# Kernel optimization log

Hardware: AMD Instinct MI355X
Metric: run time of the kernel (lower is better)

## Reference

```python
import jax, jax.numpy as jnp
import numpy as np

IMG = 512; P = 16; C = 3; DIM = 512; DEPTH = 2; HEADS = 8; HD = DIM // HEADS
MLP = 2048; W = 64; NCLS = 1000; B = 8
NPATCH = (IMG // P) ** 2          # 1024
N0 = NPATCH + 1                    # 1025 tokens incl CLS
PAD = (-N0) % (2 * W)              # pad to multiple of 2w (sliding_chunks)
N = N0 + PAD                       # 1152


def _ln(x, w, b):
    m = x.mean(-1, keepdims=True)
    v = jnp.mean((x - m) ** 2, -1, keepdims=True)
    return (x - m) * jax.lax.rsqrt(v + 1e-5) * w + b


def _heads(t):
    b, n, _ = t.shape
    return t.reshape(b, n, HEADS, HD).transpose(0, 2, 1, 3)  # b h n d


def _attn(x, mask, wq, bq, wk, bk, wv, bv, wqg, bqg, wkg, bkg, wvg, bvg):
    b, n, _ = x.shape
    sc = 1.0 / np.sqrt(HD)
    q = _heads(x @ wq + bq) * sc
    k = _heads(x @ wk + bk)
    v = _heads(x @ wv + bv)
    nc = n // W
    qc = q.reshape(b, HEADS, nc, W, HD)

    def chunk3(t):  # gather prev/self/next chunk of keys/values: b h nc 3W d
        tc = t.reshape(b, HEADS, nc, W, HD)
        z = jnp.zeros_like(tc[:, :, :1])
        prev = jnp.concatenate([z, tc[:, :, :-1]], 2)
        nxt = jnp.concatenate([tc[:, :, 1:], z], 2)
        return jnp.concatenate([prev, tc, nxt], 3)

    k3, v3 = chunk3(k), chunk3(v)
    band = jnp.einsum('bhcqd,bhckd->bhcqk', qc, k3)  # b h nc W 3W
    qi = jnp.arange(W)[:, None]
    kk = jnp.arange(3 * W)[None, :]
    rel_ok = jnp.abs(kk - W - qi) <= W               # exact +-w band
    kglob = jnp.arange(nc)[:, None, None] * W + (kk - W)[None]  # nc 1 3W
    in_rng = (kglob >= 0) & (kglob < n)
    kmask = mask[jnp.clip(kglob, 0, n - 1)]
    # keep only real local keys: exclude pad (0) and global (2, handled by gcol)
    keep = rel_ok[None] & in_rng & (kmask == 1.0)    # nc W 3W
    band = jnp.where(keep[None, None], band, -1e9)
    gcol = jnp.einsum('bhnd,bhd->bhn', q, k[:, :, 0])  # attend to global CLS key
    scores = jnp.concatenate([gcol[..., None], band.reshape(b, HEADS, n, 3 * W)], -1)
    a = jax.nn.softmax(scores, -1)                   # b h n (1+3W)
    out = jnp.einsum('bhcqk,bhckd->bhcqd', a[..., 1:].reshape(b, HEADS, nc, W, 3 * W), v3)
    out = out.reshape(b, HEADS, n, HD) + a[..., 0:1] * v[:, :, 0:1]
    # global CLS row attends to everything with its own projections
    qg0 = ((x[:, 0] @ wqg + bqg) * sc).reshape(b, HEADS, HD)
    kg = _heads(x @ wkg + bkg)
    vg = _heads(x @ wvg + bvg)
    gs = jnp.where(mask[None, None] > 0, jnp.einsum('bhd,bhnd->bhn', qg0, kg), -1e9)
    gout = jnp.einsum('bhn,bhnd->bhd', jax.nn.softmax(gs, -1), vg)
    out = out.at[:, :, 0].set(gout)
    return out.transpose(0, 2, 1, 3).reshape(b, n, DIM)


def setup_inputs():
    key = jax.random.key(0)
    ks = iter(jax.random.split(key, 20))

    def w(shape, s=0.02):
        return jax.random.normal(next(ks), shape, jnp.float32) * s

    return {
        'img': jax.random.normal(next(ks), (B, C, IMG, IMG), jnp.float32),
        'patch_w': w((P * P * C, DIM)), 'patch_b': jnp.zeros((DIM,), jnp.float32),
        'cls_tok': jax.random.uniform(next(ks), (1, 1, DIM), jnp.float32),
        'pos_emb': w((1, N0, DIM), 1.0),
        'ln1_w': jnp.ones((DEPTH, DIM), jnp.float32), 'ln1_b': jnp.zeros((DEPTH, DIM), jnp.float32),
        'wq': w((DEPTH, DIM, DIM)), 'bq': jnp.zeros((DEPTH, DIM), jnp.float32),
        'wk': w((DEPTH, DIM, DIM)), 'bk': jnp.zeros((DEPTH, DIM), jnp.float32),
        'wv': w((DEPTH, DIM, DIM)), 'bv': jnp.zeros((DEPTH, DIM), jnp.float32),
        'wqg': w((DEPTH, DIM, DIM)), 'bqg': jnp.zeros((DEPTH, DIM), jnp.float32),
        'wkg': w((DEPTH, DIM, DIM)), 'bkg': jnp.zeros((DEPTH, DIM), jnp.float32),
        'wvg': w((DEPTH, DIM, DIM)), 'bvg': jnp.zeros((DEPTH, DIM), jnp.float32),
        'ln2_w': jnp.ones((DEPTH, DIM), jnp.float32), 'ln2_b': jnp.zeros((DEPTH, DIM), jnp.float32),
        'w1': w((DEPTH, DIM, MLP)), 'b1': jnp.zeros((DEPTH, MLP), jnp.float32),
        'w2': w((DEPTH, MLP, DIM)), 'b2': jnp.zeros((DEPTH, DIM), jnp.float32),
        'head_ln_w': jnp.ones((DIM,), jnp.float32), 'head_ln_b': jnp.zeros((DIM,), jnp.float32),
        'head_w': w((DIM, NCLS)), 'head_b': jnp.zeros((NCLS,), jnp.float32),
    }


def reference(img, patch_w, patch_b, cls_tok, pos_emb, ln1_w, ln1_b, wq, bq, wk, bk,
              wv, bv, wqg, bqg, wkg, bkg, wvg, bvg, ln2_w, ln2_b, w1, b1, w2, b2,
              head_ln_w, head_ln_b, head_w, head_b):
    b = img.shape[0]
    hh = IMG // P
    # b c (h p1) (w p2) -> b (h w) (p1 p2 c)
    x = img.reshape(b, C, hh, P, hh, P).transpose(0, 2, 4, 3, 5, 1).reshape(b, hh * hh, P * P * C)
    x = x @ patch_w + patch_b
    x = jnp.concatenate([jnp.broadcast_to(cls_tok, (b, 1, DIM)), x], 1) + pos_emb
    x = jnp.pad(x, ((0, 0), (0, PAD), (0, 0)))
    mask = jnp.zeros((N,), jnp.float32).at[:N0].set(1.0).at[0].set(2.0)
    for i in range(DEPTH):
        x = x + _attn(_ln(x, ln1_w[i], ln1_b[i]), mask,
                      wq[i], bq[i], wk[i], bk[i], wv[i], bv[i],
                      wqg[i], bqg[i], wkg[i], bkg[i], wvg[i], bvg[i])
        h = jax.nn.gelu(_ln(x, ln2_w[i], ln2_b[i]) @ w1[i] + b1[i], approximate=False)
        x = x + h @ w2[i] + b2[i]
    cls = x[:, 0]  # pool='cls'
    return _ln(cls, head_ln_w, head_ln_b) @ head_w + head_b
```

## Files before the change

### kernel.cpp

```cpp
#include <hip/hip_runtime.h>
#include <hip/hip_bf16.h>
#include <math.h>

typedef __hip_bfloat16 bf16;
typedef float f32x4 __attribute__((ext_vector_type(4)));
typedef short s16x8 __attribute__((ext_vector_type(8)));
typedef unsigned int u32;

#define NB 8
#define NROW 1025
#define MTOT (NB*NROW)
#define DIMD 512
#define NHEAD 8
#define HD 64
#define MLPD 2048
#define QKVN 2560
#define JSTR 1032

__device__ __forceinline__ float b2f(short u) {
    return __builtin_bit_cast(float, (u32)(unsigned short)u << 16);
}
__device__ __forceinline__ unsigned short f2bfbits(float f) {
    __hip_bfloat16 h = __float2bfloat16(f);
    return __builtin_bit_cast(unsigned short, h);
}
__device__ __forceinline__ void g2lds16(const bf16* g, bf16* l) {
    __builtin_amdgcn_global_load_lds((const __attribute__((address_space(1))) u32*)g,
                                     (__attribute__((address_space(3))) u32*)l, 16, 0, 0);
}

__global__ __launch_bounds__(256) void transpose_cvt_L(
    const float* __restrict__ src, bf16* __restrict__ dst, int K, int N, float scale)
{
    __shared__ float t[32][33];
    const int z = blockIdx.z;
    const float* s = src + (size_t)z * K * N;
    bf16* d = dst + (size_t)z * N * K;
    const int n0 = blockIdx.x * 32, k0 = blockIdx.y * 32;
    const int tx = threadIdx.x, ty = threadIdx.y;
#pragma unroll
    for (int i = 0; i < 32; i += 8)
        t[ty + i][tx] = s[(long)(k0 + ty + i) * N + n0 + tx];
    __syncthreads();
#pragma unroll
    for (int i = 0; i < 32; i += 8)
        d[(long)(n0 + ty + i) * K + k0 + tx] = __float2bfloat16(t[tx][ty + i] * scale);
}

__global__ __launch_bounds__(256) void qkvw_t(
    const float* __restrict__ wq, const float* __restrict__ wk, const float* __restrict__ wv,
    const float* __restrict__ wkg, const float* __restrict__ wvg, bf16* __restrict__ qkvT)
{
    __shared__ float t[32][33];
    const int z = blockIdx.z, L = z / 5, s = z % 5;
    const float* srcs[5] = {wq, wk, wv, wkg, wvg};
    const float* src = srcs[s] + (size_t)L * DIMD * DIMD;
    bf16* dst = qkvT + ((size_t)L * QKVN + s * DIMD) * DIMD;
    const float scale = (s == 0) ? 0.125f : 1.f;
    const int n0 = blockIdx.x * 32, k0 = blockIdx.y * 32;
    const int tx = threadIdx.x, ty = threadIdx.y;
#pragma unroll
    for (int i = 0; i < 32; i += 8)
        t[ty + i][tx] = src[(long)(k0 + ty + i) * DIMD + n0 + tx];
    __syncthreads();
#pragma unroll
    for (int i = 0; i < 32; i += 8)
        dst[(long)(n0 + ty + i) * DIMD + k0 + tx] = __float2bfloat16(t[tx][ty + i] * scale);
}

__global__ __launch_bounds__(256) void build_bias(
    const float* __restrict__ bq, const float* __restrict__ bk, const float* __restrict__ bv,
    const float* __restrict__ bkg, const float* __restrict__ bvg, float* __restrict__ outb)
{
    int idx = blockIdx.x * 256 + threadIdx.x;
    if (idx >= 2 * QKVN) return;
    int L = idx / QKVN, c = idx % QKVN;
    int sec = c >> 9, d = c & 511;
    const float* src = (sec == 0) ? bq : (sec == 1) ? bk : (sec == 2) ? bv : (sec == 3) ? bkg : bvg;
    float v = src[L * DIMD + d];
    if (sec == 0) v *= 0.125f;
    outb[idx] = v;
}

__global__ __launch_bounds__(256) void im2col(
    const float* __restrict__ img, bf16* __restrict__ A)
{
    const int idx = blockIdx.x * 256 + threadIdx.x;
    const int pp = idx & 7;
    const int pw = (idx >> 3) & 31;
    const int py = (idx >> 8) & 15;
    const int ph = (idx >> 12) & 31;
    const int b  = idx >> 17;
    const int hh = ph * 16 + py;
    const int w  = pw * 16 + pp * 2;
    const float2 c0 = *(const float2*)(img + (((long)(b * 3 + 0) * 512 + hh) * 512 + w));
    const float2 c1 = *(const float2*)(img + (((long)(b * 3 + 1) * 512 + hh) * 512 + w));
    const float2 c2 = *(const float2*)(img + (((long)(b * 3 + 2) * 512 + hh) * 512 + w));
    const long row = (long)b * 1024 + ph * 32 + pw;
    u32* dst = (u32*)(A + row * 768 + py * 48 + pp * 6);
    dst[0] = (u32)f2bfbits(c0.x) | ((u32)f2bfbits(c1.x) << 16);
    dst[1] = (u32)f2bfbits(c2.x) | ((u32)f2bfbits(c0.y) << 16);
    dst[2] = (u32)f2bfbits(c1.y) | ((u32)f2bfbits(c2.y) << 16);
}

__global__ __launch_bounds__(256) void cls_row(
    const float* __restrict__ cls, const float* __restrict__ pos, float* __restrict__ x)
{
    const int idx = blockIdx.x * 256 + threadIdx.x;
    const int b = idx >> 9, d = idx & 511;
    x[(long)b * NROW * DIMD + d] = cls[d] + pos[d];
}

__global__ __launch_bounds__(256) void ln_fwd(
    const float* __restrict__ x, const float* __restrict__ w,
    const float* __restrict__ bb, bf16* __restrict__ y, int Mrows)
{
    const int row = blockIdx.x * 4 + (threadIdx.x >> 6);
    if (row >= Mrows) return;
    const int lane = threadIdx.x & 63;
    const float* xr = x + (long)row * DIMD + lane * 8;
    float4 a = *(const float4*)xr;
    float4 b4 = *(const float4*)(xr + 4);
    float s  = a.x + a.y + a.z + a.w + b4.x + b4.y + b4.z + b4.w;
    float sq = a.x*a.x + a.y*a.y + a.z*a.z + a.w*a.w + b4.x*b4.x + b4.y*b4.y + b4.z*b4.z + b4.w*b4.w;
#pragma unroll
    for (int o = 32; o; o >>= 1) { s += __shfl_xor(s, o); sq += __shfl_xor(sq, o); }
    float mean = s * (1.f / 512.f);
    float rstd = rsqrtf(sq * (1.f / 512.f) - mean * mean + 1e-5f);
    bf16* yr = y + (long)row * DIMD + lane * 8;
    const float* wp = w + lane * 8;
    const float* bp = bb + lane * 8;
    float vals[8] = {a.x, a.y, a.z, a.w, b4.x, b4.y, b4.z, b4.w};
#pragma unroll
    for (int u = 0; u < 8; ++u)
        yr[u] = __float2bfloat16((vals[u] - mean) * rstd * wp[u] + bp[u]);
}

template<int EPI>
__global__ __launch_bounds__(256) void gemm128(
    const bf16* __restrict__ A, const bf16* __restrict__ Bt,
    const float* __restrict__ bias,
    float* __restrict__ Cf, bf16* __restrict__ Cb,
    int M, int N, int K, const float* __restrict__ posp)
{
    __shared__ bf16 aL[2][128 * 64];
    __shared__ bf16 bL[2][128 * 64];
    const int tid = threadIdx.x, lane = tid & 63, w = tid >> 6;
    const int m0 = blockIdx.y * 128, n0 = blockIdx.x * 128;
    const int wm = w >> 1, wn = w & 1;
    f32x4 acc[4][4] = {};
    const int nk = K >> 6;
    const int srow = lane >> 3;
    const int scol = ((lane & 7) ^ srow) * 8;

#define STAGE(buf, kt) do {                                                        \
        _Pragma("unroll")                                                          \
        for (int i = 0; i < 4; ++i) {                                              \
            const int rb = i * 32 + w * 8;                                         \
            long ar = m0 + rb + srow; if (ar >= M) ar = M - 1;                     \
            g2lds16(A  + ar * (long)K + (long)(kt) * 64 + scol, &aL[buf][rb * 64]);\
            g2lds16(Bt + (long)(n0 + rb + srow) * K + (long)(kt) * 64 + scol,      \
                    &bL[buf][rb * 64]);                                            \
        } } while (0)

    STAGE(0, 0);
    __syncthreads();
    int cur = 0;
    const int fr = lane & 15;
    const int lc0 = lane >> 4;
    const int px = lane & 7;
    const int arow_b = (wm * 64 + fr) << 7;
    const int brow_b = (wn * 64 + fr) << 7;
    for (int kt = 0; kt < nk; ++kt) {
        if (kt + 1 < nk) STAGE(cur ^ 1, kt + 1);
        const char* aP = (const char*)&aL[cur][0];
        const char* bP = (const char*)&bL[cur][0];
#pragma unroll
        for (int ksub = 0; ksub < 2; ++ksub) {
            const int cb = ((ksub * 4 + lc0) ^ px) << 4;
            s16x8 af[4], bf_[4];
#pragma unroll
            for (int mi = 0; mi < 4; ++mi) af[mi]  = *(const s16x8*)(aP + arow_b + mi * 2048 + cb);
#pragma unroll
            for (int ni = 0; ni < 4; ++ni) bf_[ni] = *(const s16x8*)(bP + brow_b + ni * 2048 + cb);
#pragma unroll
            for (int mi = 0; mi < 4; ++mi)
#pragma unroll
                for (int ni = 0; ni < 4; ++ni)
                    acc[mi][ni] = __builtin_amdgcn_mfma_f32_16x16x32_bf16(af[mi], bf_[ni], acc[mi][ni], 0, 0, 0);
        }
        __syncthreads();
        cur ^= 1;
    }
#undef STAGE
    const int lr = (lane >> 4) * 4, lc = lane & 15;
#pragma unroll
    for (int mi = 0; mi < 4; ++mi) {
        const int gr0 = m0 + wm * 64 + mi * 16 + lr;
#pragma unroll
        for (int ni = 0; ni < 4; ++ni) {
            const int gc = n0 + wn * 64 + ni * 16 + lc;
            const float bv = bias[gc];
#pragma unroll
            for (int j = 0; j < 4; ++j) {
                const int gr = gr0 + j;
                if (gr < M) {
                    float v = acc[mi][ni][j] + bv;
                    if (EPI == 0) Cf[(long)gr * N + gc] = v;
                    else if (EPI == 1) Cb[(long)gr * N + gc] = __float2bfloat16(v);
                    else if (EPI == 2) {
                        float g = 0.5f * v * (1.f + erff(v * 0.70710678118f));
                        Cb[(long)gr * N + gc] = __float2bfloat16(g);
                    } else if (EPI == 3) {
                        Cf[(long)gr * N + gc] += v;
                    } else {
                        const int bb2 = gr >> 10, pidx = gr & 1023;
                        Cf[((long)bb2 * NROW + 1 + pidx) * DIMD + gc]
                            = v + posp[(long)(pidx + 1) * DIMD + gc];
                    }
                }
            }
        }
    }
}

__global__ __launch_bounds__(256) void transpose_v(
    const bf16* __restrict__ qkv, bf16* __restrict__ vT)
{
    __shared__ bf16 t[32][34];
    const int b = blockIdx.z;
    const int j0 = blockIdx.x * 32, d0 = blockIdx.y * 32;
    const int tx = threadIdx.x, ty = threadIdx.y;
#pragma unroll
    for (int i = 0; i < 32; i += 8) {
        int j = j0 + ty + i; if (j > 1024) j = 1024;
        t[ty + i][tx] = qkv[((long)b * NROW + j) * QKVN + 1024 + d0 + tx];
    }
    __syncthreads();
#pragma unroll
    for (int i = 0; i < 32; i += 8) {
        int j = j0 + tx;
        if (j <= 1024)
            vT[((long)b * 512 + d0 + ty + i) * JSTR + j] = t[tx][ty + i];
    }
}

__global__ __launch_bounds__(256) void band_attn_mfma(
    const bf16* __restrict__ qkv, const bf16* __restrict__ vT, float* __restrict__ x)
{
    __shared__ bf16 Kl[208 * 72];
    __shared__ bf16 Vt[64 * 192];
    __shared__ bf16 Pl[4 * 16 * 192];
    __shared__ float V0l[64];
    const int c = blockIdx.x, h = blockIdx.y, b = blockIdx.z;
    const int tid = threadIdx.x, lane = tid & 63, w = tid >> 6;
    const int qi0 = 1 + c * 64, jbase = qi0 - 64;
    const long rowb = (long)b * NROW;
    const int hoff = h * HD;

    for (int task = tid; task < 208 * 8; task += 256) {
        const int d8 = task & 7, r = task >> 3;
        s16x8 val = {};
        if (r <= 192) {
            int j = (r < 192) ? (jbase + r) : 0;
            j = j < 0 ? 0 : (j > 1024 ? 1024 : j);
            val = *(const s16x8*)(qkv + (rowb + j) * QKVN + 512 + hoff + d8 * 8);
        }
        *(s16x8*)(Kl + r * 72 + d8 * 8) = val;
    }
    for (int task = tid; task < 64 * 24; task += 256) {
        const int kc = task % 24, d = task / 24;
        int j0 = jbase + kc * 8;
        j0 = j0 < 0 ? 0 : (j0 > 1017 ? 1017 : j0);
        s16x8 v = *(const s16x8*)(vT + ((long)(b * 512 + hoff + d)) * JSTR + j0);
        const int bo = (d * 384 + kc * 16) ^ ((d & 7) << 4);
        *(s16x8*)((char*)Vt + bo) = v;
    }
    if (tid < 64) V0l[tid] = __bfloat162float(qkv[rowb * QKVN + 1024 + hoff + tid]);

    const int q = lane & 15, g = lane >> 4;
    const int qg = w * 16 + q;
    s16x8 qf0, qf1;
    {
        const bf16* qp = qkv + (rowb + qi0 + qg) * QKVN + hoff + g * 8;
        qf0 = *(const s16x8*)qp;
        qf1 = *(const s16x8*)(qp + 32);
    }
    __syncthreads();

    f32x4 sc[13] = {};
#pragma unroll
    for (int nt = 0; nt < 13; ++nt) {
        const bf16* kp = Kl + (nt * 16 + q) * 72 + g * 8;
        s16x8 k0 = *(const s16x8*)kp;
        s16x8 k1 = *(const s16x8*)(kp + 32);
        sc[nt] = __builtin_amdgcn_mfma_f32_16x16x32_bf16(k0, qf0, sc[nt], 0, 0, 0);
        sc[nt] = __builtin_amdgcn_mfma_f32_16x16x32_bf16(k1, qf1, sc[nt], 0, 0, 0);
    }

    const int lo_ = (qg > 1 - jbase) ? qg : 1 - jbase;
    const int hi_ = (qg + 128 < 1024 - jbase) ? qg + 128 : 1024 - jbase;
    float m = -1e30f;
#pragma unroll
    for (int nt = 0; nt < 12; ++nt)
#pragma unroll
        for (int j = 0; j < 4; ++j) {
            const int slot = nt * 16 + g * 4 + j;
            float s = (slot >= lo_ && slot <= hi_) ? sc[nt][j] : -1e9f;
            sc[nt][j] = s;
            m = fmaxf(m, s);
        }
#pragma unroll
    for (int j = 0; j < 4; ++j) {
        float s = (g == 0 && j == 0) ? sc[12][j] : -1e9f;
        sc[12][j] = s;
        m = fmaxf(m, s);
    }
    m = fmaxf(m, __shfl_xor(m, 16));
    m = fmaxf(m, __shfl_xor(m, 32));
    float sum = 0.f;
#pragma unroll
    for (int nt = 0; nt < 13; ++nt)
#pragma unroll
        for (int j = 0; j < 4; ++j) {
            float p = __expf(sc[nt][j] - m);
            sc[nt][j] = p;
            sum += p;
        }
    sum += __shfl_xor(sum, 16);
    sum += __shfl_xor(sum, 32);
    const float inv = 1.f / sum;
    const float a0 = __shfl(sc[12][0], q);

    char* plw = (char*)Pl + w * 6144;
#pragma unroll
    for (int nt = 0; nt < 12; ++nt) {
        u32 lo2 = (u32)f2bfbits(sc[nt][0]) | ((u32)f2bfbits(sc[nt][1]) << 16);
        u32 hi2 = (u32)f2bfbits(sc[nt][2]) | ((u32)f2bfbits(sc[nt][3]) << 16);
        const int bo = (q * 384 + (nt * 16 + g * 4) * 2) ^ ((q & 7) << 4);
        *(uint2*)(plw + bo) = make_uint2(lo2, hi2);
    }
    __syncthreads();

    f32x4 ac[4] = {};
#pragma unroll
    for (int ks = 0; ks < 6; ++ks) {
        const int pbo = (q * 384 + (ks * 32 + g * 8) * 2) ^ ((q & 7) << 4);
        s16x8 pf = *(const s16x8*)(plw + pbo);
#pragma unroll
        for (int mt = 0; mt < 4; ++mt) {
            const int d = mt * 16 + q;
            const int vbo = ((d * 192 + ks * 32 + g * 8) * 2) ^ ((d & 7) << 4);
            s16x8 vf = *(const s16x8*)((char*)Vt + vbo);
            ac[mt] = __builtin_amdgcn_mfma_f32_16x16x32_bf16(vf, pf, ac[mt], 0, 0, 0);
        }
    }

    float* xr = x + (rowb + qi0 + qg) * DIMD + hoff;
#pragma unroll
    for (int mt = 0; mt < 4; ++mt) {
        const int d0 = mt * 16 + g * 4;
        float4 prev = *(float4*)(xr + d0);
        prev.x += (ac[mt][0] + a0 * V0l[d0 + 0]) * inv;
        prev.y += (ac[mt][1] + a0 * V0l[d0 + 1]) * inv;
        prev.z += (ac[mt][2] + a0 * V0l[d0 + 2]) * inv;
        prev.w += (ac[mt][3] + a0 * V0l[d0 + 3]) * inv;
        *(float4*)(xr + d0) = prev;
    }
}

__global__ __launch_bounds__(256) void qg_proj(
    const bf16* __restrict__ ybf, const float* __restrict__ wqg,
    const float* __restrict__ bqg, float* __restrict__ qg_all)
{
    __shared__ float y0[512];
    const int b = blockIdx.x, tid = threadIdx.x;
    const long rowb = (long)b * NROW;
    for (int d = tid; d < 512; d += 256) y0[d] = __bfloat162float(ybf[rowb * DIMD + d]);
    __syncthreads();
    const int c = blockIdx.y * 256 + tid;
    float a = 0.f;
#pragma unroll 8
    for (int kk = 0; kk < 512; ++kk) a += y0[kk] * wqg[(long)kk * DIMD + c];
    qg_all[b * DIMD + c] = (a + bqg[c]) * 0.125f;
}

__global__ __launch_bounds__(256) void glob_av(
    const float* __restrict__ qg_all, const bf16* __restrict__ qkv, float* __restrict__ x)
{
    __shared__ float qgs[64];
    __shared__ float red[256];
    __shared__ float P[1025];
    const int hh = blockIdx.x, b = blockIdx.y;
    const int tid = threadIdx.x;
    const long rowb = (long)b * NROW;
    const int hoff = hh * HD;
    if (tid < 64) qgs[tid] = qg_all[b * DIMD + hoff + tid];
    __syncthreads();
    const int dd = tid & 63, part = tid >> 6;
    for (int j = tid; j < 1025; j += 256) {
        const bf16* kr = qkv + (rowb + j) * QKVN + 1536 + hoff;
        float s = 0.f;
#pragma unroll
        for (int c8 = 0; c8 < 8; ++c8) {
            s16x8 kv = *(const s16x8*)(kr + c8 * 8);
#pragma unroll
            for (int e = 0; e < 8; ++e) s += qgs[c8 * 8 + e] * b2f(kv[e]);
        }
        P[j] = s;
    }
    __syncthreads();
    float lm = -1e30f;
    for (int j = tid; j < 1025; j += 256) lm = fmaxf(lm, P[j]);
    red[tid] = lm; __syncthreads();
    for (int st = 128; st; st >>= 1) { if (tid < st) red[tid] = fmaxf(red[tid], red[tid + st]); __syncthreads(); }
    const float mx = red[0]; __syncthreads();
    float ls = 0.f;
    for (int j = tid; j < 1025; j += 256) { float e = __expf(P[j] - mx); P[j] = e; ls += e; }
    red[tid] = ls; __syncthreads();
    for (int st = 128; st; st >>= 1) { if (tid < st) red[tid] += red[tid + st]; __syncthreads(); }
    const float inv = 1.f / red[0];
    __syncthreads();
    float acc = 0.f;
#pragma unroll 4
    for (int j = part; j < 1025; j += 4)
        acc += P[j] * __bfloat162float(qkv[(rowb + j) * QKVN + 2048 + hoff + dd]);
    red[tid] = acc;
    __syncthreads();
    if (part == 0)
        x[rowb * DIMD + hoff + dd] += (red[dd] + red[64 + dd] + red[128 + dd] + red[192 + dd]) * inv;
}

__global__ __launch_bounds__(512) void lncls(
    const float* __restrict__ x, const float* __restrict__ lw,
    const float* __restrict__ lb, float* __restrict__ out)
{
    const int b = threadIdx.x >> 6, lane = threadIdx.x & 63;
    const int d0 = lane * 8;
    const float* xr = x + (long)b * NROW * DIMD + d0;
    float4 a = *(const float4*)xr;
    float4 b4 = *(const float4*)(xr + 4);
    float s  = a.x + a.y + a.z + a.w + b4.x + b4.y + b4.z + b4.w;
    float sq = a.x*a.x + a.y*a.y + a.z*a.z + a.w*a.w + b4.x*b4.x + b4.y*b4.y + b4.z*b4.z + b4.w*b4.w;
#pragma unroll
    for (int o = 32; o; o >>= 1) { s += __shfl_xor(s, o); sq += __shfl_xor(sq, o); }
    const float mean = s * (1.f / 512.f);
    const float rstd = rsqrtf(sq * (1.f / 512.f) - mean * mean + 1e-5f);
    float vals[8] = {a.x, a.y, a.z, a.w, b4.x, b4.y, b4.z, b4.w};
#pragma unroll
    for (int u = 0; u < 8; ++u)
        out[b * DIMD + d0 + u] = (vals[u] - mean) * rstd * lw[d0 + u] + lb[d0 + u];
}

__global__ __launch_bounds__(128) void head_gemv(
    const float* __restrict__ lnc, const float* __restrict__ hw,
    const float* __restrict__ hb, float* __restrict__ out)
{
    const int idx = blockIdx.x * 128 + threadIdx.x;
    if (idx >= NB * 1000) return;
    const int b = idx / 1000, cc = idx - b * 1000;
    const float* lr = lnc + b * DIMD;
    float a = hb[cc];
#pragma unroll 8
    for (int kk = 0; kk < 512; ++kk) a += lr[kk] * hw[(long)kk * 1000 + cc];
    out[idx] = a;
}

extern "C" void kernel_launch(void* const* d_in, const int* in_sizes, int n_in,
                              void* d_out, int out_size, void* d_ws, size_t ws_size,
                              hipStream_t stream)
{
    const float* img     = (const float*)d_in[0];
    const float* patch_w = (const float*)d_in[1];
    const float* patch_b = (const float*)d_in[2];
    const float* cls_tok = (const float*)d_in[3];
    const float* pos_emb = (const float*)d_in[4];
    const float* ln1_w   = (const float*)d_in[5];
    const float* ln1_b   = (const float*)d_in[6];
    const float* wq  = (const float*)d_in[7];
    const float* bq  = (const float*)d_in[8];
    const float* wk  = (const float*)d_in[9];
    const float* bk  = (const float*)d_in[10];
    const float* wv  = (const float*)d_in[11];
    const float* bv  = (const float*)d_in[12];
    const float* wqg = (const float*)d_in[13];
    const float* bqg = (const float*)d_in[14];
    const float* wkg = (const float*)d_in[15];
    const float* bkg = (const float*)d_in[16];
    const float* wvg = (const float*)d_in[17];
    const float* bvg = (const float*)d_in[18];
    const float* ln2_w = (const float*)d_in[19];
    const float* ln2_b = (const float*)d_in[20];
    const float* w1 = (const float*)d_in[21];
    const float* b1 = (const float*)d_in[22];
    const float* w2 = (const float*)d_in[23];
    const float* b2 = (const float*)d_in[24];
    const float* hlw = (const float*)d_in[25];
    const float* hlb = (const float*)d_in[26];
    const float* hw  = (const float*)d_in[27];
    const float* hb  = (const float*)d_in[28];

    char* wsb = (char*)d_ws;
    size_t o = 0;
    auto carve = [&](size_t n) { size_t r = o; o += (n + 255) & ~(size_t)255; return r; };
    float* x    = (float*)(wsb + carve((size_t)MTOT * DIMD * 4));
    bf16*  ybf  = (bf16*) (wsb + carve((size_t)MTOT * DIMD * 2));
    bf16*  qkv  = (bf16*) (wsb + carve((size_t)MTOT * QKVN * 2));
    bf16*  hbuf = (bf16*) (wsb + carve((size_t)MTOT * MLPD * 2));
    bf16*  vT   = (bf16*) (wsb + carve((size_t)NB * 512 * JSTR * 2));
    bf16*  acol = (bf16*) (wsb + carve((size_t)8192 * 768 * 2));
    bf16*  pwt  = (bf16*) (wsb + carve((size_t)512 * 768 * 2));
    bf16*  qkvT = (bf16*) (wsb + carve((size_t)2 * QKVN * DIMD * 2));
    bf16*  w1t  = (bf16*) (wsb + carve((size_t)2 * MLPD * DIMD * 2));
    bf16*  w2t  = (bf16*) (wsb + carve((size_t)2 * DIMD * MLPD * 2));
    float* catb = (float*)(wsb + carve((size_t)2 * QKVN * 4));
    float* qg_all = (float*)(wsb + carve((size_t)NB * DIMD * 4));
    float* lnc    = (float*)(wsb + carve((size_t)NB * DIMD * 4));
    (void)ws_size; (void)in_sizes; (void)n_in; (void)out_size;

    dim3 tb(32, 8);
    transpose_cvt_L<<<dim3(16, 24, 1), tb, 0, stream>>>(patch_w, pwt, 768, 512, 1.f);
    qkvw_t<<<dim3(16, 16, 10), tb, 0, stream>>>(wq, wk, wv, wkg, wvg, qkvT);
    transpose_cvt_L<<<dim3(64, 16, 2), tb, 0, stream>>>(w1, w1t, DIMD, MLPD, 1.f);
    transpose_cvt_L<<<dim3(16, 64, 2), tb, 0, stream>>>(w2, w2t, MLPD, DIMD, 1.f);
    build_bias<<<20, 256, 0, stream>>>(bq, bk, bv, bkg, bvg, catb);

    im2col<<<4096, 256, 0, stream>>>(img, acol);
    gemm128<4><<<dim3(4, 64), 256, 0, stream>>>(
        acol, pwt, patch_b, x, nullptr, 8192, 512, 768, pos_emb);
    cls_row<<<16, 256, 0, stream>>>(cls_tok, pos_emb, x);

    for (int L = 0; L < 2; ++L) {
        ln_fwd<<<2050, 256, 0, stream>>>(x, ln1_w + L * DIMD, ln1_b + L * DIMD, ybf, MTOT);
        gemm128<1><<<dim3(QKVN/128, 65), 256, 0, stream>>>(
            ybf, qkvT + (size_t)L * QKVN * DIMD, catb + L * QKVN, nullptr, qkv, MTOT, QKVN, DIMD, nullptr);
        transpose_v<<<dim3(33, 16, NB), tb, 0, stream>>>(qkv, vT);
        band_attn_mfma<<<dim3(16, NHEAD, NB), 256, 0, stream>>>(qkv, vT, x);
        qg_proj<<<dim3(NB, 2), 256, 0, stream>>>(
            ybf, wqg + (size_t)L * DIMD * DIMD, bqg + L * DIMD, qg_all);
        glob_av<<<dim3(NHEAD, NB), 256, 0, stream>>>(qg_all, qkv, x);
        ln_fwd<<<2050, 256, 0, stream>>>(x, ln2_w + L * DIMD, ln2_b + L * DIMD, ybf, MTOT);
        gemm128<2><<<dim3(MLPD/128, 65), 256, 0, stream>>>(
            ybf, w1t + (size_t)L * MLPD * DIMD, b1 + L * MLPD, nullptr, hbuf, MTOT, MLPD, DIMD, nullptr);
        gemm128<3><<<dim3(DIMD/128, 65), 256, 0, stream>>>(
            hbuf, w2t + (size_t)L * DIMD * MLPD, b2 + L * DIMD, x, nullptr, MTOT, DIMD, MLPD, nullptr);
    }
    lncls<<<1, 512, 0, stream>>>(x, hlw, hlb, lnc);
    head_gemv<<<63, 128, 0, stream>>>(lnc, hw, hb, (float*)d_out);
}
```

Baseline: 582.8 us.

## Fuse V transpose into QKV GEMM epilogue and merge global attention into band kernel

```diff
diff --git a/kernel.cpp b/kernel.cpp
--- a/kernel.cpp
+++ b/kernel.cpp
@@ -6,6 +6,7 @@
 typedef float f32x4 __attribute__((ext_vector_type(4)));
 typedef short s16x8 __attribute__((ext_vector_type(8)));
 typedef unsigned int u32;
+typedef unsigned long long u64;
 
 #define NB 8
 #define NROW 1025
@@ -141,7 +142,7 @@
     const bf16* __restrict__ A, const bf16* __restrict__ Bt,
     const float* __restrict__ bias,
     float* __restrict__ Cf, bf16* __restrict__ Cb,
-    int M, int N, int K, const float* __restrict__ posp)
+    int M, int N, int K, const float* __restrict__ posp, bf16* __restrict__ vTout)
 {
     __shared__ bf16 aL[2][128 * 64];
     __shared__ bf16 bL[2][128 * 64];
@@ -201,22 +202,53 @@
         for (int ni = 0; ni < 4; ++ni) {
             const int gc = n0 + wn * 64 + ni * 16 + lc;
             const float bv = bias[gc];
-#pragma unroll
-            for (int j = 0; j < 4; ++j) {
-                const int gr = gr0 + j;
-                if (gr < M) {
-                    float v = acc[mi][ni][j] + bv;
-                    if (EPI == 0) Cf[(long)gr * N + gc] = v;
-                    else if (EPI == 1) Cb[(long)gr * N + gc] = __float2bfloat16(v);
-                    else if (EPI == 2) {
-                        float g = 0.5f * v * (1.f + erff(v * 0.70710678118f));
-                        Cb[(long)gr * N + gc] = __float2bfloat16(g);
-                    } else if (EPI == 3) {
-                        Cf[(long)gr * N + gc] += v;
+            if (EPI == 1) {
+                unsigned short pk[4];
+#pragma unroll
+                for (int j = 0; j < 4; ++j) {
+                    const int gr = gr0 + j;
+                    if (gr < M) {
+                        bf16 hv = __float2bfloat16(acc[mi][ni][j] + bv);
+                        Cb[(long)gr * N + gc] = hv;
+                        pk[j] = __builtin_bit_cast(unsigned short, hv);
+                    } else pk[j] = 0;
+                }
+                if (gc >= 1024 && gc < 1536) {
+                    const int d = gc - 1024;
+                    const int bb2 = gr0 / NROW, jj = gr0 - bb2 * NROW;
+                    if (jj <= 1021 && gr0 + 3 < M) {
+                        u64 pack =  (u64)pk[0] | ((u64)pk[1] << 16)
+                                 | ((u64)pk[2] << 32) | ((u64)pk[3] << 48);
+                        *(u64*)&vTout[((long)bb2 * 512 + d) * JSTR + jj] = pack;
                     } else {
-                        const int bb2 = gr >> 10, pidx = gr & 1023;
-                        Cf[((long)bb2 * NROW + 1 + pidx) * DIMD + gc]
-                            = v + posp[(long)(pidx + 1) * DIMD + gc];
+#pragma unroll
+                        for (int j = 0; j < 4; ++j) {
+                            const int gr = gr0 + j;
+                            if (gr < M) {
+                                const int b3 = gr / NROW, j3 = gr - b3 * NROW;
+                                vTout[((long)b3 * 512 + d) * JSTR + j3] =
+                                    __builtin_bit_cast(bf16, pk[j]);
+                            }
+                        }
+                    }
+                }
+            } else {
+#pragma unroll
+                for (int j = 0; j < 4; ++j) {
+                    const int gr = gr0 + j;
+                    if (gr < M) {
+                        float v = acc[mi][ni][j] + bv;
+                        if (EPI == 0) Cf[(long)gr * N + gc] = v;
+                        else if (EPI == 2) {
+                            float g = 0.5f * v * (1.f + erff(v * 0.70710678118f));
+                            Cb[(long)gr * N + gc] = __float2bfloat16(g);
+                        } else if (EPI == 3) {
+                            Cf[(long)gr * N + gc] += v;
+                        } else {
+                            const int bb2 = gr >> 10, pidx = gr & 1023;
+                            Cf[((long)bb2 * NROW + 1 + pidx) * DIMD + gc]
+                                = v + posp[(long)(pidx + 1) * DIMD + gc];
+                        }
                     }
                 }
             }
@@ -224,29 +256,10 @@
     }
 }
 
-__global__ __launch_bounds__(256) void transpose_v(
-    const bf16* __restrict__ qkv, bf16* __restrict__ vT)
-{
-    __shared__ bf16 t[32][34];
-    const int b = blockIdx.z;
-    const int j0 = blockIdx.x * 32, d0 = blockIdx.y * 32;
-    const int tx = threadIdx.x, ty = threadIdx.y;
-#pragma unroll
-    for (int i = 0; i < 32; i += 8) {
-        int j = j0 + ty + i; if (j > 1024) j = 1024;
-        t[ty + i][tx] = qkv[((long)b * NROW + j) * QKVN + 1024 + d0 + tx];
-    }
-    __syncthreads();
-#pragma unroll
-    for (int i = 0; i < 32; i += 8) {
-        int j = j0 + tx;
-        if (j <= 1024)
-            vT[((long)b * 512 + d0 + ty + i) * JSTR + j] = t[tx][ty + i];
-    }
-}
-
-__global__ __launch_bounds__(256) void band_attn_mfma(
-    const bf16* __restrict__ qkv, const bf16* __restrict__ vT, float* __restrict__ x)
+__global__ __launch_bounds__(256) void band_glob_attn(
+    const bf16* __restrict__ qkv, const bf16* __restrict__ vT,
+    const bf16* __restrict__ ybf, const float* __restrict__ wqg,
+    const float* __restrict__ bqg, float* __restrict__ x)
 {
     __shared__ bf16 Kl[208 * 72];
     __shared__ bf16 Vt[64 * 192];
@@ -254,9 +267,64 @@
     __shared__ float V0l[64];
     const int c = blockIdx.x, h = blockIdx.y, b = blockIdx.z;
     const int tid = threadIdx.x, lane = tid & 63, w = tid >> 6;
-    const int qi0 = 1 + c * 64, jbase = qi0 - 64;
     const long rowb = (long)b * NROW;
     const int hoff = h * HD;
+
+    if (c == 16) {
+        float* gsh  = (float*)Kl;
+        float* y0   = gsh;
+        float* P    = gsh + 512;
+        float* qgs  = gsh + 1537;
+        float* redx = gsh + 1601;
+        for (int d = tid; d < 512; d += 256) y0[d] = __bfloat162float(ybf[rowb * DIMD + d]);
+        __syncthreads();
+        const int dd = tid & 63, part = tid >> 6;
+        {
+            float a = 0.f;
+            for (int kk = part; kk < 512; kk += 4)
+                a += y0[kk] * wqg[(long)kk * DIMD + hoff + dd];
+            redx[tid] = a;
+        }
+        __syncthreads();
+        if (part == 0)
+            qgs[dd] = (redx[dd] + redx[64 + dd] + redx[128 + dd] + redx[192 + dd]
+                       + bqg[hoff + dd]) * 0.125f;
+        __syncthreads();
+        for (int j = tid; j < 1025; j += 256) {
+            const bf16* kr = qkv + (rowb + j) * QKVN + 1536 + hoff;
+            float s = 0.f;
+#pragma unroll
+            for (int c8 = 0; c8 < 8; ++c8) {
+                s16x8 kv = *(const s16x8*)(kr + c8 * 8);
+#pragma unroll
+                for (int e = 0; e < 8; ++e) s += qgs[c8 * 8 + e] * b2f(kv[e]);
+            }
+            P[j] = s;
+        }
+        __syncthreads();
+        float lm = -1e30f;
+        for (int j = tid; j < 1025; j += 256) lm = fmaxf(lm, P[j]);
+        redx[tid] = lm; __syncthreads();
+        for (int st = 128; st; st >>= 1) { if (tid < st) redx[tid] = fmaxf(redx[tid], redx[tid + st]); __syncthreads(); }
+        const float mx = redx[0]; __syncthreads();
+        float ls = 0.f;
+        for (int j = tid; j < 1025; j += 256) { float e = __expf(P[j] - mx); P[j] = e; ls += e; }
+        redx[tid] = ls; __syncthreads();
+        for (int st = 128; st; st >>= 1) { if (tid < st) redx[tid] += redx[tid + st]; __syncthreads(); }
+        const float invg = 1.f / redx[0];
+        __syncthreads();
+        float accg = 0.f;
+#pragma unroll 4
+        for (int j = part; j < 1025; j += 4)
+            accg += P[j] * __bfloat162float(qkv[(rowb + j) * QKVN + 2048 + hoff + dd]);
+        redx[tid] = accg;
+        __syncthreads();
+        if (part == 0)
+            x[rowb * DIMD + hoff + dd] += (redx[dd] + redx[64 + dd] + redx[128 + dd] + redx[192 + dd]) * invg;
+        return;
+    }
+
+    const int qi0 = 1 + c * 64, jbase = qi0 - 64;
 
     for (int task = tid; task < 208 * 8; task += 256) {
         const int d8 = task & 7, r = task >> 3;
@@ -367,68 +435,6 @@
         prev.w += (ac[mt][3] + a0 * V0l[d0 + 3]) * inv;
         *(float4*)(xr + d0) = prev;
     }
-}
-
-__global__ __launch_bounds__(256) void qg_proj(
-    const bf16* __restrict__ ybf, const float* __restrict__ wqg,
-    const float* __restrict__ bqg, float* __restrict__ qg_all)
-{
-    __shared__ float y0[512];
-    const int b = blockIdx.x, tid = threadIdx.x;
-    const long rowb = (long)b * NROW;
-    for (int d = tid; d < 512; d += 256) y0[d] = __bfloat162float(ybf[rowb * DIMD + d]);
-    __syncthreads();
-    const int c = blockIdx.y * 256 + tid;
-    float a = 0.f;
-#pragma unroll 8
-    for (int kk = 0; kk < 512; ++kk) a += y0[kk] * wqg[(long)kk * DIMD + c];
-    qg_all[b * DIMD + c] = (a + bqg[c]) * 0.125f;
-}
-
-__global__ __launch_bounds__(256) void glob_av(
-    const float* __restrict__ qg_all, const bf16* __restrict__ qkv, float* __restrict__ x)
-{
-    __shared__ float qgs[64];
-    __shared__ float red[256];
-    __shared__ float P[1025];
-    const int hh = blockIdx.x, b = blockIdx.y;
-    const int tid = threadIdx.x;
-    const long rowb = (long)b * NROW;
-    const int hoff = hh * HD;
-    if (tid < 64) qgs[tid] = qg_all[b * DIMD + hoff + tid];
-    __syncthreads();
-    const int dd = tid & 63, part = tid >> 6;
-    for (int j = tid; j < 1025; j += 256) {
-        const bf16* kr = qkv + (rowb + j) * QKVN + 1536 + hoff;
-        float s = 0.f;
-#pragma unroll
-        for (int c8 = 0; c8 < 8; ++c8) {
-            s16x8 kv = *(const s16x8*)(kr + c8 * 8);
-#pragma unroll
-            for (int e = 0; e < 8; ++e) s += qgs[c8 * 8 + e] * b2f(kv[e]);
-        }
-        P[j] = s;
-    }
-    __syncthreads();
-    float lm = -1e30f;
-    for (int j = tid; j < 1025; j += 256) lm = fmaxf(lm, P[j]);
-    red[tid] = lm; __syncthreads();
-    for (int st = 128; st; st >>= 1) { if (tid < st) red[tid] = fmaxf(red[tid], red[tid + st]); __syncthreads(); }
-    const float mx = red[0]; __syncthreads();
-    float ls = 0.f;
-    for (int j = tid; j < 1025; j += 256) { float e = __expf(P[j] - mx); P[j] = e; ls += e; }
-    red[tid] = ls; __syncthreads();
-    for (int st = 128; st; st >>= 1) { if (tid < st) red[tid] += red[tid + st]; __syncthreads(); }
-    const float inv = 1.f / red[0];
-    __syncthreads();
-    float acc = 0.f;
-#pragma unroll 4
-    for (int j = part; j < 1025; j += 4)
-        acc += P[j] * __bfloat162float(qkv[(rowb + j) * QKVN + 2048 + hoff + dd]);
-    red[tid] = acc;
-    __syncthreads();
-    if (part == 0)
-        x[rowb * DIMD + hoff + dd] += (red[dd] + red[64 + dd] + red[128 + dd] + red[192 + dd]) * inv;
 }
 
 __global__ __launch_bounds__(512) void lncls(
@@ -514,8 +520,7 @@
     bf16*  w1t  = (bf16*) (wsb + carve((size_t)2 * MLPD * DIMD * 2));
     bf16*  w2t  = (bf16*) (wsb + carve((size_t)2 * DIMD * MLPD * 2));
     float* catb = (float*)(wsb + carve((size_t)2 * QKVN * 4));
-    float* qg_all = (float*)(wsb + carve((size_t)NB * DIMD * 4));
-    float* lnc    = (float*)(wsb + carve((size_t)NB * DIMD * 4));
+    float* lnc  = (float*)(wsb + carve((size_t)NB * DIMD * 4));
     (void)ws_size; (void)in_sizes; (void)n_in; (void)out_size;
 
     dim3 tb(32, 8);
@@ -527,23 +532,23 @@
 
     im2col<<<4096, 256, 0, stream>>>(img, acol);
     gemm128<4><<<dim3(4, 64), 256, 0, stream>>>(
-        acol, pwt, patch_b, x, nullptr, 8192, 512, 768, pos_emb);
+        acol, pwt, patch_b, x, nullptr, 8192, 512, 768, pos_emb, nullptr);
     cls_row<<<16, 256, 0, stream>>>(cls_tok, pos_emb, x);
 
     for (int L = 0; L < 2; ++L) {
         ln_fwd<<<2050, 256, 0, stream>>>(x, ln1_w + L * DIMD, ln1_b + L * DIMD, ybf, MTOT);
         gemm128<1><<<dim3(QKVN/128, 65), 256, 0, stream>>>(
-            ybf, qkvT + (size_t)L * QKVN * DIMD, catb + L * QKVN, nullptr, qkv, MTOT, QKVN, DIMD, nullptr);
-        transpose_v<<<dim3(33, 16, NB), tb, 0, stream>>>(qkv, vT);
-        band_attn_mfma<<<dim3(16, NHEAD, NB), 256, 0, stream>>>(qkv, vT, x);
-        qg_proj<<<dim3(NB, 2), 256, 0, stream>>>(
-            ybf, wqg + (size_t)L * DIMD * DIMD, bqg + L * DIMD, qg_all);
-        glob_av<<<dim3(NHEAD, NB), 256, 0, stream>>>(qg_all, qkv, x);
+            ybf, qkvT + (size_t)L * QKVN * DIMD, catb + L * QKVN, nullptr, qkv,
+            MTOT, QKVN, DIMD, nullptr, vT);
+        band_glob_attn<<<dim3(17, NHEAD, NB), 256, 0, stream>>>(
+            qkv, vT, ybf, wqg + (size_t)L * DIMD * DIMD, bqg + L * DIMD, x);
         ln_fwd<<<2050, 256, 0, stream>>>(x, ln2_w + L * DIMD, ln2_b + L * DIMD, ybf, MTOT);
         gemm128<2><<<dim3(MLPD/128, 65), 256, 0, stream>>>(
-            ybf, w1t + (size_t)L * MLPD * DIMD, b1 + L * MLPD, nullptr, hbuf, MTOT, MLPD, DIMD, nullptr);
+            ybf, w1t + (size_t)L * MLPD * DIMD, b1 + L * MLPD, nullptr, hbuf,
+            MTOT, MLPD, DIMD, nullptr, nullptr);
         gemm128<3><<<dim3(DIMD/128, 65), 256, 0, stream>>>(
-            hbuf, w2t + (size_t)L * DIMD * MLPD, b2 + L * DIMD, x, nullptr, MTOT, DIMD, MLPD, nullptr);
+            hbuf, w2t + (size_t)L * DIMD * MLPD, b2 + L * DIMD, x, nullptr,
+            MTOT, DIMD, MLPD, nullptr, nullptr);
     }
     lncls<<<1, 512, 0, stream>>>(x, hlw, hlb, lnc);
     head_gemv<<<63, 128, 0, stream>>>(lnc, hw, hb, (float*)d_out);
```

Measured after the change: 578.6 us. No clear change (-0.7%).
